# Kernel optimization log

Measured on AMD Instinct MI355X. Metric: run time of the kernel, lower is better.

## Reference

```python
import jax, jax.numpy as jnp
import numpy as np

D = 1024      # d_model
H = 16        # n_head
DH = D // H   # d_head = 64
DFF = 4 * D   # 4096
B, T = 1, 4096
EPS = 1e-5


def _layernorm(x, scale, bias):
    mu = jnp.mean(x, axis=-1, keepdims=True)
    var = jnp.mean(jnp.square(x - mu), axis=-1, keepdims=True)
    return (x - mu) * jax.lax.rsqrt(var + EPS) * scale + bias


def setup_inputs() -> dict:
    key = jax.random.key(0)
    ks = jax.random.split(key, 8)
    s = 0.02
    return {
        "x": jax.random.normal(ks[0], (B, T, D), jnp.float32),
        "ln1_scale": jnp.ones((D,), jnp.float32),
        "ln1_bias": jnp.zeros((D,), jnp.float32),
        "W_attn": jax.random.normal(ks[1], (D, 3 * D), jnp.float32) * s,
        "b_attn": jnp.zeros((3 * D,), jnp.float32),
        "W_proj": jax.random.normal(ks[2], (D, D), jnp.float32) * s,
        "b_proj": jnp.zeros((D,), jnp.float32),
        "ln2_scale": jnp.ones((D,), jnp.float32),
        "ln2_bias": jnp.zeros((D,), jnp.float32),
        "W_fc": jax.random.normal(ks[3], (D, DFF), jnp.float32) * s,
        "b_fc": jnp.zeros((DFF,), jnp.float32),
        "W_fc2": jax.random.normal(ks[4], (DFF, D), jnp.float32) * s,
        "b_fc2": jnp.zeros((D,), jnp.float32),
    }


def reference(x, ln1_scale, ln1_bias, W_attn, b_attn, W_proj, b_proj,
              ln2_scale, ln2_bias, W_fc, b_fc, W_fc2, b_fc2):
    Bx, Tx, C = x.shape
    # --- attention branch ---
    h = _layernorm(x, ln1_scale, ln1_bias)
    qkv = h @ W_attn + b_attn                      # [B,T,3D]
    q, k, v = jnp.split(qkv, 3, axis=-1)
    q = q.reshape(Bx, Tx, H, DH).transpose(0, 2, 1, 3)  # [B,H,T,dh]
    k = k.reshape(Bx, Tx, H, DH).transpose(0, 2, 1, 3)
    v = v.reshape(Bx, Tx, H, DH).transpose(0, 2, 1, 3)
    att = jnp.einsum('bhqd,bhkd->bhqk', q, k) * (1.0 / jnp.sqrt(DH))
    causal = jnp.tril(jnp.ones((Tx, Tx), dtype=jnp.bool_))[None, None]
    att = jnp.where(causal, att, -jnp.inf)
    att = jax.nn.softmax(att, axis=-1)
    y = jnp.einsum('bhqk,bhkd->bhqd', att, v)      # [B,H,T,dh]
    y = y.transpose(0, 2, 1, 3).reshape(Bx, Tx, C)
    y = y @ W_proj + b_proj
    x = x + y
    # --- MLP branch ---
    h2 = _layernorm(x, ln2_scale, ln2_bias)
    m = jax.nn.gelu(h2 @ W_fc + b_fc)              # approximate gelu (flax default)
    m = m @ W_fc2 + b_fc2
    return x + m
```

## Files before the change

kernel.cpp:

```cpp
#include <hip/hip_runtime.h>
#include <hip/hip_bf16.h>

typedef short bf16x8 __attribute__((ext_vector_type(8)));
typedef float f32x4 __attribute__((ext_vector_type(4)));
typedef unsigned short u16;
typedef unsigned int u32;

#define TSEQ 4096
#define DMODEL 1024
#define NHEAD 16
#define DHEAD 64
#define DFF 4096

__device__ __forceinline__ u16 f2bf(float f) {
    u32 u = __builtin_bit_cast(u32, f);
    u32 lsb = (u >> 16) & 1u;
    u += 0x7fffu + lsb;
    return (u16)(u >> 16);
}

__device__ __forceinline__ float exp2_hw(float x) {
    float r;
    asm("v_exp_f32 %0, %1" : "=v"(r) : "v"(x));
    return r;
}

__device__ __forceinline__ float rcp_hw(float x) {
    float r;
    asm("v_rcp_f32 %0, %1" : "=v"(r) : "v"(x));
    return r;
}

__device__ __forceinline__ u32 cvt_pk_bf16(float a, float b) {
    u32 r;
    asm("v_cvt_pk_bf16_f32 %0, %1, %2" : "=v"(r) : "v"(a), "v"(b));
    return r;
}

__device__ __forceinline__ void gload_lds16(const u16* g, u16* l) {
    __builtin_amdgcn_global_load_lds(
        (const __attribute__((address_space(1))) u32*)g,
        (__attribute__((address_space(3))) u32*)l, 16, 0, 0);
}

__device__ __forceinline__ void transpose_tile(
    const float* __restrict__ W, u16* __restrict__ Wt, int K, int N, int bx, int by,
    float (*tile)[65])
{
    const int t = threadIdx.x;
    const int c = t & 63, r4 = t >> 6;
    const int col0 = bx * 64;
    const int row0 = by * 64;
#pragma unroll
    for (int p = 0; p < 16; p++) {
        const int r = 4 * p + r4;
        tile[r][c] = W[(size_t)(row0 + r) * N + col0 + c];
    }
    __syncthreads();
#pragma unroll
    for (int p = 0; p < 16; p++) {
        const int r = 4 * p + r4;
        Wt[(size_t)(col0 + r) * K + row0 + c] = f2bf(tile[c][r]);
    }
}

__device__ __forceinline__ void ln_rows(
    const float* __restrict__ x, const float* __restrict__ sc,
    const float* __restrict__ bi, u16* __restrict__ out, int blk)
{
    const int lane = threadIdx.x & 63;
    const int row = blk * 4 + (threadIdx.x >> 6);
    const float* xr = x + (size_t)row * DMODEL;
    float4 v[4];
    float s = 0.f, s2 = 0.f;
#pragma unroll
    for (int q = 0; q < 4; q++) {
        v[q] = *(const float4*)(xr + 4 * (lane + 64 * q));
        s  += v[q].x + v[q].y + v[q].z + v[q].w;
        s2 += v[q].x * v[q].x + v[q].y * v[q].y + v[q].z * v[q].z + v[q].w * v[q].w;
    }
#pragma unroll
    for (int off = 1; off < 64; off <<= 1) {
        s  += __shfl_xor(s, off);
        s2 += __shfl_xor(s2, off);
    }
    const float mu = s * (1.f / DMODEL);
    const float rstd = rsqrtf(s2 * (1.f / DMODEL) - mu * mu + 1e-5f);
#pragma unroll
    for (int q = 0; q < 4; q++) {
        const int c = 4 * (lane + 64 * q);
        const float4 scv = *(const float4*)(sc + c);
        const float4 biv = *(const float4*)(bi + c);
        ushort4 ov;
        ov.x = f2bf((v[q].x - mu) * rstd * scv.x + biv.x);
        ov.y = f2bf((v[q].y - mu) * rstd * scv.y + biv.y);
        ov.z = f2bf((v[q].z - mu) * rstd * scv.z + biv.z);
        ov.w = f2bf((v[q].w - mu) * rstd * scv.w + biv.w);
        *(ushort4*)(out + (size_t)row * DMODEL + c) = ov;
    }
}

__global__ __launch_bounds__(256)
void prep_kernel(const float* __restrict__ x, const float* __restrict__ ln1_s,
                 const float* __restrict__ ln1_b, u16* __restrict__ h,
                 const float* __restrict__ W_attn, u16* __restrict__ WtAttn,
                 const float* __restrict__ W_proj, u16* __restrict__ WtProj,
                 const float* __restrict__ W_fc,   u16* __restrict__ WtFc,
                 const float* __restrict__ W_fc2,  u16* __restrict__ WtFc2)
{
    __shared__ float tile[64][65];
    int b = blockIdx.x;
    if (b < 1024) { ln_rows(x, ln1_s, ln1_b, h, b); return; }
    b -= 1024;
    if (b < 768)  { transpose_tile(W_attn, WtAttn, 1024, 3072, b % 48, b / 48, tile); return; }
    b -= 768;
    if (b < 256)  { transpose_tile(W_proj, WtProj, 1024, 1024, b % 16, b / 16, tile); return; }
    b -= 256;
    if (b < 1024) { transpose_tile(W_fc,   WtFc,   1024, 4096, b % 64, b / 64, tile); return; }
    b -= 1024;
    transpose_tile(W_fc2, WtFc2, 4096, 1024, b % 16, b / 16, tile);
}

__global__ __launch_bounds__(256)
void v_transpose_kernel(const u16* __restrict__ qkv, u16* __restrict__ Vtg)
{
    __shared__ u16 tile[64][72];
    const int t = threadIdx.x;
    const int hh = blockIdx.y, t0 = blockIdx.x * 64;
#pragma unroll
    for (int p = 0; p < 2; p++) {
        const int L = p * 2048 + t * 8;
        const int r = L >> 6, c = L & 63;
        const bf16x8 v = *(const bf16x8*)(qkv + (size_t)(t0 + r) * 3072 + 2048 + hh * 64 + c);
#pragma unroll
        for (int i = 0; i < 8; i++) tile[c + i][r] = (u16)v[i];
    }
    __syncthreads();
#pragma unroll
    for (int p = 0; p < 2; p++) {
        const int L = p * 2048 + t * 8;
        const int d = L >> 6, c = L & 63;
        bf16x8 v;
#pragma unroll
        for (int i = 0; i < 8; i++) v[i] = (short)tile[d][c + i];
        *(bf16x8*)(Vtg + (size_t)(hh * 64 + d) * TSEQ + t0 + c) = v;
    }
}

__global__ __launch_bounds__(256)
void ln_kernel(const float* __restrict__ x, const float* __restrict__ sc,
               const float* __restrict__ bi, u16* __restrict__ out)
{
    ln_rows(x, sc, bi, out, blockIdx.x);
}

template<int BN, int GELU_F, int OUT_BF16, int HAS_RES, int HAS_BIAS, int FUSE_Z1 = 0>
__global__ __launch_bounds__(256)
void gemm_kernel(const u16* __restrict__ A, int lda,
                 const u16* __restrict__ Bt, int ldb,
                 const float* __restrict__ bias, const float* __restrict__ res,
                 u16* __restrict__ outb, float* __restrict__ outf0,
                 float* __restrict__ outf1, int M, int N, int Kblk)
{
    constexpr int MI = (BN == 128) ? 4 : 2;
    __shared__ u16 Alds[128 * 64];
    __shared__ u16 Blds[BN * 64];
    const int t = threadIdx.x;
    const int lane = t & 63, w = t >> 6;
    const int g = lane >> 4, fr = lane & 15;
    const int m0 = blockIdx.y * 128, n0 = blockIdx.x * BN;
    const size_t koff = (size_t)blockIdx.z * Kblk;
    const int rowbase = (BN == 128) ? (w >> 1) * 64 : w * 32;
    const int colbase = (BN == 128) ? (w & 1) * 64 : 0;
    float* outf = blockIdx.z ? outf1 : outf0;

    f32x4 zero4 = {0.f, 0.f, 0.f, 0.f};
    f32x4 acc[MI][4];
#pragma unroll
    for (int i = 0; i < MI; i++)
#pragma unroll
        for (int j = 0; j < 4; j++) acc[i][j] = zero4;

    for (int k0 = 0; k0 < Kblk; k0 += 64) {
        __syncthreads();
#pragma unroll
        for (int p = 0; p < 4; p++) {
            const int c = p * 256 + t;
            const int r = c >> 3, j = (c & 7) ^ (r & 7);
            gload_lds16(A + (size_t)(m0 + r) * lda + koff + k0 + j * 8, Alds + c * 8);
        }
#pragma unroll
        for (int p = 0; p < (BN == 128 ? 4 : 2); p++) {
            const int c = p * 256 + t;
            const int r = c >> 3, j = (c & 7) ^ (r & 7);
            gload_lds16(Bt + (size_t)(n0 + r) * ldb + koff + k0 + j * 8, Blds + c * 8);
        }
        __syncthreads();

#pragma unroll
        for (int ks = 0; ks < 2; ks++) {
            bf16x8 af[MI], bfr[4];
#pragma unroll
            for (int i = 0; i < MI; i++)
                af[i] = *(const bf16x8*)(Alds + (rowbase + i * 16 + fr) * 64 + (((ks * 4 + g) ^ (fr & 7)) * 8));
#pragma unroll
            for (int j = 0; j < 4; j++)
                bfr[j] = *(const bf16x8*)(Blds + (colbase + j * 16 + fr) * 64 + (((ks * 4 + g) ^ (fr & 7)) * 8));
#pragma unroll
            for (int i = 0; i < MI; i++)
#pragma unroll
                for (int j = 0; j < 4; j++)
                    acc[i][j] = __builtin_amdgcn_mfma_f32_16x16x32_bf16(af[i], bfr[j], acc[i][j], 0, 0, 0);
        }
    }

    const bool fuse = FUSE_Z1 && (blockIdx.z == 1);
#pragma unroll
    for (int j = 0; j < 4; j++) {
        const int col = n0 + colbase + j * 16 + fr;
        float bv = 0.f;
        if (HAS_BIAS) bv = bias[col];
        if (FUSE_Z1 && fuse) bv = bias[col];
#pragma unroll
        for (int i = 0; i < MI; i++) {
#pragma unroll
            for (int r = 0; r < 4; r++) {
                const int row = m0 + rowbase + i * 16 + g * 4 + r;
                float v = acc[i][j][r] + bv;
                if (GELU_F) {
                    const float q = 0.7978845608028654f * (v + 0.044715f * v * v * v);
                    const float e = exp2_hw(fminf(q, 30.f) * 2.8853900817779268f);
                    v = v * e * rcp_hw(e + 1.0f);
                }
                if (HAS_RES) v += res[(size_t)row * N + col];
                if (FUSE_Z1 && fuse) v += res[(size_t)row * N + col];
                if (OUT_BF16) outb[(size_t)row * N + col] = f2bf(v);
                else          outf[(size_t)row * N + col] = v;
            }
        }
    }
}

__global__ __launch_bounds__(512, 2)
void gemm256_kernel(const u16* __restrict__ A, const u16* __restrict__ Bt,
                    const float* __restrict__ bias, u16* __restrict__ outb,
                    int M, int N, int K)
{
    __shared__ u16 Alds[256 * 64];
    __shared__ u16 Blds[128 * 64];
    const int t = threadIdx.x;
    const int lane = t & 63, w = t >> 6;
    const int g = lane >> 4, fr = lane & 15;
    const int m0 = blockIdx.y * 256, n0 = blockIdx.x * 128;
    const int rowbase = (w >> 1) * 64;
    const int colbase = (w & 1) * 64;

    f32x4 zero4 = {0.f, 0.f, 0.f, 0.f};
    f32x4 acc[4][4];
#pragma unroll
    for (int i = 0; i < 4; i++)
#pragma unroll
        for (int j = 0; j < 4; j++) acc[i][j] = zero4;

    for (int k0 = 0; k0 < K; k0 += 64) {
        __syncthreads();
#pragma unroll
        for (int p = 0; p < 4; p++) {
            const int c = p * 512 + t;
            const int r = c >> 3, j = (c & 7) ^ (r & 7);
            gload_lds16(A + (size_t)(m0 + r) * K + k0 + j * 8, Alds + c * 8);
        }
#pragma unroll
        for (int p = 0; p < 2; p++) {
            const int c = p * 512 + t;
            const int r = c >> 3, j = (c & 7) ^ (r & 7);
            gload_lds16(Bt + (size_t)(n0 + r) * K + k0 + j * 8, Blds + c * 8);
        }
        __syncthreads();

#pragma unroll
        for (int ks = 0; ks < 2; ks++) {
            bf16x8 af[4], bfr[4];
#pragma unroll
            for (int i = 0; i < 4; i++)
                af[i] = *(const bf16x8*)(Alds + (rowbase + i * 16 + fr) * 64 + (((ks * 4 + g) ^ (fr & 7)) * 8));
#pragma unroll
            for (int j = 0; j < 4; j++)
                bfr[j] = *(const bf16x8*)(Blds + (colbase + j * 16 + fr) * 64 + (((ks * 4 + g) ^ (fr & 7)) * 8));
#pragma unroll
            for (int i = 0; i < 4; i++)
#pragma unroll
                for (int j = 0; j < 4; j++)
                    acc[i][j] = __builtin_amdgcn_mfma_f32_16x16x32_bf16(af[i], bfr[j], acc[i][j], 0, 0, 0);
        }
    }

#pragma unroll
    for (int j = 0; j < 4; j++) {
        const int col = n0 + colbase + j * 16 + fr;
        const float bv = bias[col];
#pragma unroll
        for (int i = 0; i < 4; i++) {
#pragma unroll
            for (int r = 0; r < 4; r++) {
                const int row = m0 + rowbase + i * 16 + g * 4 + r;
                float v = acc[i][j][r] + bv;
                const float q = 0.7978845608028654f * (v + 0.044715f * v * v * v);
                const float e = exp2_hw(fminf(q, 30.f) * 2.8853900817779268f);
                v = v * e * rcp_hw(e + 1.0f);
                outb[(size_t)row * N + col] = f2bf(v);
            }
        }
    }
}

__global__ __launch_bounds__(256)
void fc2_merge_kernel(float* __restrict__ out, const float* __restrict__ part)
{
    const int i = blockIdx.x * 256 + threadIdx.x;
    const float4 o = ((const float4*)out)[i];
    const float4 p = ((const float4*)part)[i];
    float4 v;
    v.x = o.x + p.x;
    v.y = o.y + p.y;
    v.z = o.z + p.z;
    v.w = o.w + p.w;
    ((float4*)out)[i] = v;
}

__device__ __forceinline__ void softmax_update(
    const f32x4 st[4], bool diag, int klim, int g, int fr,
    float& mrow, float& lrow, f32x4 o[4], u16* Pl)
{
    const float ninf = -__builtin_inff();
    const float C = 0.125f * 1.4426950408889634f;
    float av[4][4];
#pragma unroll
    for (int ct = 0; ct < 4; ct++)
#pragma unroll
        for (int r = 0; r < 4; r++) {
            float aa = st[ct][r];
            if (diag && (ct * 16 + g * 4 + r) > klim) aa = ninf;
            av[ct][r] = aa;
        }
    float m0 = fmaxf(fmaxf(av[0][0], av[0][1]), fmaxf(av[0][2], av[0][3]));
    float m1 = fmaxf(fmaxf(av[1][0], av[1][1]), fmaxf(av[1][2], av[1][3]));
    float m2 = fmaxf(fmaxf(av[2][0], av[2][1]), fmaxf(av[2][2], av[2][3]));
    float m3 = fmaxf(fmaxf(av[3][0], av[3][1]), fmaxf(av[3][2], av[3][3]));
    float vm = fmaxf(fmaxf(m0, m1), fmaxf(m2, m3));
    vm = fmaxf(vm, __shfl_xor(vm, 16));
    vm = fmaxf(vm, __shfl_xor(vm, 32));
    const float mn = (vm <= mrow + 64.f) ? mrow : vm;
    const float mnC = mn * C;
    float rs = 0.f;
#pragma unroll
    for (int ct = 0; ct < 4; ct++) {
        const float p0 = exp2_hw(__builtin_fmaf(av[ct][0], C, -mnC));
        const float p1 = exp2_hw(__builtin_fmaf(av[ct][1], C, -mnC));
        const float p2 = exp2_hw(__builtin_fmaf(av[ct][2], C, -mnC));
        const float p3 = exp2_hw(__builtin_fmaf(av[ct][3], C, -mnC));
        rs += (p0 + p1) + (p2 + p3);
        uint2 pk;
        pk.x = cvt_pk_bf16(p0, p1);
        pk.y = cvt_pk_bf16(p2, p3);
        const int chunk = ct * 2 + (g >> 1);
        const int addr = fr * 64 + ((chunk ^ (fr & 7)) * 8) + (g & 1) * 4;
        *(uint2*)(Pl + addr) = pk;
    }
    rs += __shfl_xor(rs, 16);
    rs += __shfl_xor(rs, 32);
    const float sc = exp2_hw((mrow - mn) * C);
    lrow = __builtin_fmaf(lrow, sc, rs);
    const bool nores = (mn == mrow);
    mrow = mn;
    if (!__all(nores)) {
        float scb[4];
#pragma unroll
        for (int j = 0; j < 4; j++) scb[j] = __shfl(sc, g * 4 + j);
#pragma unroll
        for (int dt = 0; dt < 4; dt++)
#pragma unroll
            for (int j = 0; j < 4; j++) o[dt][j] *= scb[j];
    }
}

__global__ __launch_bounds__(512, 4)
void attn_kernel(const u16* __restrict__ qkv, const u16* __restrict__ Vtg,
                 u16* __restrict__ y)
{
    __shared__ u16 Klds[2][128 * 64];
    __shared__ u16 Vlds[2][64 * 128];
    __shared__ u16 Plds[8][16 * 64];
    const int t = threadIdx.x, lane = t & 63, w = t >> 6;
    const int g = lane >> 4, fr = lane & 15;
    const int wv = w & 3, grp = w >> 2;
    const int hh = blockIdx.y;
    const int ii = blockIdx.x;
    const int ntB = 64 - ii;
    const int qAw = ii * 64 + wv * 16;
    const int qBw = (63 - ii) * 64 + wv * 16;

    bf16x8 aqA[2], aqB[2];
#pragma unroll
    for (int s = 0; s < 2; s++) {
        aqA[s] = *(const bf16x8*)(qkv + (size_t)(qAw + fr) * 3072 + hh * 64 + s * 32 + g * 8);
        aqB[s] = *(const bf16x8*)(qkv + (size_t)(qBw + fr) * 3072 + hh * 64 + s * 32 + g * 8);
    }

    f32x4 zero4 = {0.f, 0.f, 0.f, 0.f};
    f32x4 oA[4] = {zero4, zero4, zero4, zero4};
    f32x4 oB[4] = {zero4, zero4, zero4, zero4};
    const float ninf = -__builtin_inff();
    float mA = ninf, lA = 0.f, mB = ninf, lB = 0.f;

    const int cK0 = t, cK1 = t + 512;
    const int rK0 = cK0 >> 3, jK0 = (cK0 & 7) ^ (rK0 & 7);
    const int rK1 = cK1 >> 3, jK1 = (cK1 & 7) ^ (rK1 & 7);
    const int rv0 = cK0 >> 4, cj0 = cK0 & 15;
    const int jv0 = (cj0 & 8) | ((cj0 & 7) ^ (rv0 & 7));
    const int rv1 = cK1 >> 4, cj1 = cK1 & 15;
    const int jv1 = (cj1 & 8) | ((cj1 & 7) ^ (rv1 & 7));
    const u16* gk0 = qkv + (size_t)rK0 * 3072 + 1024 + hh * 64 + jK0 * 8;
    const u16* gk1 = qkv + (size_t)rK1 * 3072 + 1024 + hh * 64 + jK1 * 8;
    const u16* gv0 = Vtg + (size_t)(hh * 64 + rv0) * TSEQ + jv0 * 8;
    const u16* gv1 = Vtg + (size_t)(hh * 64 + rv1) * TSEQ + jv1 * 8;

#define STAGE(buf, k0) do { \
        gload_lds16(gk0 + (size_t)(k0) * 3072, Klds[buf] + cK0 * 8); \
        gload_lds16(gk1 + (size_t)(k0) * 3072, Klds[buf] + cK1 * 8); \
        gload_lds16(gv0 + (k0), Vlds[buf] + cK0 * 8); \
        gload_lds16(gv1 + (k0), Vlds[buf] + cK1 * 8); \
    } while (0)

    const int nIter = (65 - ii) >> 1;
    STAGE(0, 0);

    int cur = 0;
    for (int j = 0; j < nIter; j++) {
        __syncthreads();
        if (j + 1 < nIter) STAGE(cur ^ 1, (j + 1) * 128);

        const int kt = 2 * j + grp;
        const bool aB = kt < ntB;
        const bool aA = kt <= ii;
        if (aB | aA) {
            const u16* Kl = Klds[cur] + grp * (64 * 64);
            const u16* Vl = Vlds[cur];
            const int klim = wv * 16 + fr;

            f32x4 stA[4] = {zero4, zero4, zero4, zero4};
            f32x4 stB[4] = {zero4, zero4, zero4, zero4};
#pragma unroll
            for (int ct = 0; ct < 4; ct++) {
#pragma unroll
                for (int ds = 0; ds < 2; ds++) {
                    const bf16x8 bk = *(const bf16x8*)(Kl + (ct * 16 + fr) * 64 + (((ds * 4 + g) ^ (fr & 7)) * 8));
                    if (aB) stB[ct] = __builtin_amdgcn_mfma_f32_16x16x32_bf16(bk, aqB[ds], stB[ct], 0, 0, 0);
                    if (aA) stA[ct] = __builtin_amdgcn_mfma_f32_16x16x32_bf16(bk, aqA[ds], stA[ct], 0, 0, 0);
                }
            }

            if (aB) {
                softmax_update(stB, kt == ntB - 1, klim, g, fr, mB, lB, oB, Plds[w]);
                __builtin_amdgcn_s_waitcnt(0xc07f);
#pragma unroll
                for (int kkh = 0; kkh < 2; kkh++) {
                    const bf16x8 pa = *(const bf16x8*)(&Plds[w][fr * 64 + (((kkh * 4 + g) ^ (fr & 7)) * 8)]);
#pragma unroll
                    for (int dt = 0; dt < 4; dt++) {
                        const int cc = grp * 8 + kkh * 4 + g;
                        const bf16x8 bv = *(const bf16x8*)(Vl + (dt * 16 + fr) * 128 + (((cc & 8) | ((cc & 7) ^ (fr & 7))) * 8));
                        oB[dt] = __builtin_amdgcn_mfma_f32_16x16x32_bf16(pa, bv, oB[dt], 0, 0, 0);
                    }
                }
            }
            if (aA) {
                softmax_update(stA, kt == ii, klim, g, fr, mA, lA, oA, Plds[w]);
                __builtin_amdgcn_s_waitcnt(0xc07f);
#pragma unroll
                for (int kkh = 0; kkh < 2; kkh++) {
                    const bf16x8 pa = *(const bf16x8*)(&Plds[w][fr * 64 + (((kkh * 4 + g) ^ (fr & 7)) * 8)]);
#pragma unroll
                    for (int dt = 0; dt < 4; dt++) {
                        const int cc = grp * 8 + kkh * 4 + g;
                        const bf16x8 bv = *(const bf16x8*)(Vl + (dt * 16 + fr) * 128 + (((cc & 8) | ((cc & 7) ^ (fr & 7))) * 8));
                        oA[dt] = __builtin_amdgcn_mfma_f32_16x16x32_bf16(pa, bv, oA[dt], 0, 0, 0);
                    }
                }
            }
        }
        cur ^= 1;
    }
#undef STAGE

    __syncthreads();
    float* Of = (float*)&Klds[0][0];
    float2* Ml = (float2*)&Vlds[0][0];
    const float C = 0.125f * 1.4426950408889634f;
    if (grp == 1) {
#pragma unroll
        for (int dt = 0; dt < 4; dt++)
#pragma unroll
            for (int jq = 0; jq < 4; jq++) {
                Of[((wv * 2 + 0) * 16 + g * 4 + jq) * 64 + dt * 16 + fr] = oA[dt][jq];
                Of[((wv * 2 + 1) * 16 + g * 4 + jq) * 64 + dt * 16 + fr] = oB[dt][jq];
            }
        if (g == 0) {
            Ml[(wv * 2 + 0) * 16 + fr] = make_float2(mA, lA);
            Ml[(wv * 2 + 1) * 16 + fr] = make_float2(mB, lB);
        }
    }
    __syncthreads();
    if (grp == 0) {
#pragma unroll
        for (int jq = 0; jq < 4; jq++) {
            {
                const float m0 = __shfl(mA, g * 4 + jq), l0 = __shfl(lA, g * 4 + jq);
                const float2 ml1 = Ml[(wv * 2 + 0) * 16 + g * 4 + jq];
                const float mm = fmaxf(m0, ml1.x);
                const float s0 = exp2_hw((m0 - mm) * C);
                const float s1 = exp2_hw((ml1.x - mm) * C);
                const float rl = rcp_hw(__builtin_fmaf(l0, s0, ml1.y * s1));
#pragma unroll
                for (int dt = 0; dt < 4; dt++) {
                    const float o1 = Of[((wv * 2 + 0) * 16 + g * 4 + jq) * 64 + dt * 16 + fr];
                    y[(size_t)(qAw + g * 4 + jq) * DMODEL + hh * 64 + dt * 16 + fr] =
                        f2bf((oA[dt][jq] * s0 + o1 * s1) * rl);
                }
            }
            {
                const float m0 = __shfl(mB, g * 4 + jq), l0 = __shfl(lB, g * 4 + jq);
                const float2 ml1 = Ml[(wv * 2 + 1) * 16 + g * 4 + jq];
                const float mm = fmaxf(m0, ml1.x);
                const float s0 = exp2_hw((m0 - mm) * C);
                const float s1 = exp2_hw((ml1.x - mm) * C);
                const float rl = rcp_hw(__builtin_fmaf(l0, s0, ml1.y * s1));
#pragma unroll
                for (int dt = 0; dt < 4; dt++) {
                    const float o1 = Of[((wv * 2 + 1) * 16 + g * 4 + jq) * 64 + dt * 16 + fr];
                    y[(size_t)(qBw + g * 4 + jq) * DMODEL + hh * 64 + dt * 16 + fr] =
                        f2bf((oB[dt][jq] * s0 + o1 * s1) * rl);
                }
            }
        }
    }
}

extern "C" void kernel_launch(void* const* d_in, const int* in_sizes, int n_in,
                              void* d_out, int out_size, void* d_ws, size_t ws_size,
                              hipStream_t stream)
{
    const float* x      = (const float*)d_in[0];
    const float* ln1_s  = (const float*)d_in[1];
    const float* ln1_b  = (const float*)d_in[2];
    const float* W_attn = (const float*)d_in[3];
    const float* b_attn = (const float*)d_in[4];
    const float* W_proj = (const float*)d_in[5];
    const float* b_proj = (const float*)d_in[6];
    const float* ln2_s  = (const float*)d_in[7];
    const float* ln2_b  = (const float*)d_in[8];
    const float* W_fc   = (const float*)d_in[9];
    const float* b_fc   = (const float*)d_in[10];
    const float* W_fc2  = (const float*)d_in[11];
    const float* b_fc2  = (const float*)d_in[12];
    float* out = (float*)d_out;

    char* ws = (char*)d_ws;
    u16* WtAttn = (u16*)ws; ws += (size_t)3072 * 1024 * 2;
    u16* WtProj = (u16*)ws; ws += (size_t)1024 * 1024 * 2;
    u16* WtFc   = (u16*)ws; ws += (size_t)4096 * 1024 * 2;
    u16* WtFc2  = (u16*)ws; ws += (size_t)1024 * 4096 * 2;
    u16* bufA   = (u16*)ws; ws += (size_t)4096 * 1024 * 2;
    u16* bufB   = (u16*)ws; ws += (size_t)4096 * 4096 * 2;
    float* x1   = (float*)ws; ws += (size_t)4096 * 1024 * 4;
    u16* Vtg    = (u16*)x1;
    float* P0   = (float*)d_ws;

    prep_kernel<<<4096, 256, 0, stream>>>(x, ln1_s, ln1_b, bufA,
                                          W_attn, WtAttn, W_proj, WtProj,
                                          W_fc, WtFc, W_fc2, WtFc2);

    gemm_kernel<128, 0, 1, 0, 1><<<dim3(24, 32, 1), 256, 0, stream>>>(
        bufA, 1024, WtAttn, 1024, b_attn, nullptr, bufB, nullptr, nullptr, 4096, 3072, 1024);
    v_transpose_kernel<<<dim3(TSEQ / 64, NHEAD), 256, 0, stream>>>(bufB, Vtg);
    attn_kernel<<<dim3(32, NHEAD), 512, 0, stream>>>(bufB, Vtg, bufA);
    gemm_kernel<64, 0, 0, 1, 1><<<dim3(16, 32, 1), 256, 0, stream>>>(
        bufA, 1024, WtProj, 1024, b_proj, x, nullptr, x1, nullptr, 4096, 1024, 1024);

    ln_kernel<<<TSEQ / 4, 256, 0, stream>>>(x1, ln2_s, ln2_b, bufA);
    gemm256_kernel<<<dim3(32, 16), 512, 0, stream>>>(
        bufA, WtFc, b_fc, bufB, 4096, 4096, 1024);
    gemm_kernel<128, 0, 0, 0, 0, 1><<<dim3(8, 32, 2), 256, 0, stream>>>(
        bufB, 4096, WtFc2, 4096, b_fc2, x1, nullptr, P0, out, 4096, 1024, 2048);
    fc2_merge_kernel<<<4096, 256, 0, stream>>>(out, P0);
}
```

Baseline: 280.9 us.

## Split-K the output projection, fuse merge into LN2, add MFMA priority hints

The output projection GEMM now uses 128-wide tiles with a two-way split-K. One partial goes into x1 together with the residual and bias, and the other goes into a scratch buffer. A new ln_merge kernel adds the two partials, writes x1 back, and computes the second layernorm in one pass using a single-pass mean and variance. In the attention kernel, causal masking is moved out of the softmax so it only runs on diagonal tiles, and s_setprio raises wave priority around the MFMA sections. This trades extra partial-buffer traffic for better CU occupancy on the projection GEMM, and the single-pass variance can lose some numerical precision.

```diff
diff --git a/kernel.cpp b/kernel.cpp
--- a/kernel.cpp
+++ b/kernel.cpp
@@ -148,10 +148,46 @@
 }
 
 __global__ __launch_bounds__(256)
-void ln_kernel(const float* __restrict__ x, const float* __restrict__ sc,
-               const float* __restrict__ bi, u16* __restrict__ out)
-{
-    ln_rows(x, sc, bi, out, blockIdx.x);
+void ln_merge_kernel(float* __restrict__ x1, const float* __restrict__ part,
+                     const float* __restrict__ sc, const float* __restrict__ bi,
+                     u16* __restrict__ out)
+{
+    const int lane = threadIdx.x & 63;
+    const int row = blockIdx.x * 4 + (threadIdx.x >> 6);
+    float* xr = x1 + (size_t)row * DMODEL;
+    const float* pr = part + (size_t)row * DMODEL;
+    float4 v[4];
+    float s = 0.f, s2 = 0.f;
+#pragma unroll
+    for (int q = 0; q < 4; q++) {
+        const int c = 4 * (lane + 64 * q);
+        const float4 a = *(const float4*)(xr + c);
+        const float4 p = *(const float4*)(pr + c);
+        v[q].x = a.x + p.x; v[q].y = a.y + p.y;
+        v[q].z = a.z + p.z; v[q].w = a.w + p.w;
+        *(float4*)(xr + c) = v[q];
+        s  += v[q].x + v[q].y + v[q].z + v[q].w;
+        s2 += v[q].x * v[q].x + v[q].y * v[q].y + v[q].z * v[q].z + v[q].w * v[q].w;
+    }
+#pragma unroll
+    for (int off = 1; off < 64; off <<= 1) {
+        s  += __shfl_xor(s, off);
+        s2 += __shfl_xor(s2, off);
+    }
+    const float mu = s * (1.f / DMODEL);
+    const float rstd = rsqrtf(s2 * (1.f / DMODEL) - mu * mu + 1e-5f);
+#pragma unroll
+    for (int q = 0; q < 4; q++) {
+        const int c = 4 * (lane + 64 * q);
+        const float4 scv = *(const float4*)(sc + c);
+        const float4 biv = *(const float4*)(bi + c);
+        ushort4 ov;
+        ov.x = f2bf((v[q].x - mu) * rstd * scv.x + biv.x);
+        ov.y = f2bf((v[q].y - mu) * rstd * scv.y + biv.y);
+        ov.z = f2bf((v[q].z - mu) * rstd * scv.z + biv.z);
+        ov.w = f2bf((v[q].w - mu) * rstd * scv.w + biv.w);
+        *(ushort4*)(out + (size_t)row * DMODEL + c) = ov;
+    }
 }
 
 template<int BN, int GELU_F, int OUT_BF16, int HAS_RES, int HAS_BIAS, int FUSE_Z1 = 0>
@@ -328,25 +364,25 @@
     ((float4*)out)[i] = v;
 }
 
+__device__ __forceinline__ void mask_diag(f32x4 st[4], int klim, int g)
+{
+    const float ninf = -__builtin_inff();
+#pragma unroll
+    for (int ct = 0; ct < 4; ct++)
+#pragma unroll
+        for (int r = 0; r < 4; r++)
+            if (ct * 16 + g * 4 + r > klim) st[ct][r] = ninf;
+}
+
 __device__ __forceinline__ void softmax_update(
-    const f32x4 st[4], bool diag, int klim, int g, int fr,
+    const f32x4 st[4], int g, int fr,
     float& mrow, float& lrow, f32x4 o[4], u16* Pl)
 {
-    const float ninf = -__builtin_inff();
     const float C = 0.125f * 1.4426950408889634f;
-    float av[4][4];
-#pragma unroll
-    for (int ct = 0; ct < 4; ct++)
-#pragma unroll
-        for (int r = 0; r < 4; r++) {
-            float aa = st[ct][r];
-            if (diag && (ct * 16 + g * 4 + r) > klim) aa = ninf;
-            av[ct][r] = aa;
-        }
-    float m0 = fmaxf(fmaxf(av[0][0], av[0][1]), fmaxf(av[0][2], av[0][3]));
-    float m1 = fmaxf(fmaxf(av[1][0], av[1][1]), fmaxf(av[1][2], av[1][3]));
-    float m2 = fmaxf(fmaxf(av[2][0], av[2][1]), fmaxf(av[2][2], av[2][3]));
-    float m3 = fmaxf(fmaxf(av[3][0], av[3][1]), fmaxf(av[3][2], av[3][3]));
+    float m0 = fmaxf(fmaxf(st[0][0], st[0][1]), fmaxf(st[0][2], st[0][3]));
+    float m1 = fmaxf(fmaxf(st[1][0], st[1][1]), fmaxf(st[1][2], st[1][3]));
+    float m2 = fmaxf(fmaxf(st[2][0], st[2][1]), fmaxf(st[2][2], st[2][3]));
+    float m3 = fmaxf(fmaxf(st[3][0], st[3][1]), fmaxf(st[3][2], st[3][3]));
     float vm = fmaxf(fmaxf(m0, m1), fmaxf(m2, m3));
     vm = fmaxf(vm, __shfl_xor(vm, 16));
     vm = fmaxf(vm, __shfl_xor(vm, 32));
@@ -355,10 +391,10 @@
     float rs = 0.f;
 #pragma unroll
     for (int ct = 0; ct < 4; ct++) {
-        const float p0 = exp2_hw(__builtin_fmaf(av[ct][0], C, -mnC));
-        const float p1 = exp2_hw(__builtin_fmaf(av[ct][1], C, -mnC));
-        const float p2 = exp2_hw(__builtin_fmaf(av[ct][2], C, -mnC));
-        const float p3 = exp2_hw(__builtin_fmaf(av[ct][3], C, -mnC));
+        const float p0 = exp2_hw(__builtin_fmaf(st[ct][0], C, -mnC));
+        const float p1 = exp2_hw(__builtin_fmaf(st[ct][1], C, -mnC));
+        const float p2 = exp2_hw(__builtin_fmaf(st[ct][2], C, -mnC));
+        const float p3 = exp2_hw(__builtin_fmaf(st[ct][3], C, -mnC));
         rs += (p0 + p1) + (p2 + p3);
         uint2 pk;
         pk.x = cvt_pk_bf16(p0, p1);
@@ -450,6 +486,7 @@
 
             f32x4 stA[4] = {zero4, zero4, zero4, zero4};
             f32x4 stB[4] = {zero4, zero4, zero4, zero4};
+            __builtin_amdgcn_s_setprio(1);
 #pragma unroll
             for (int ct = 0; ct < 4; ct++) {
 #pragma unroll
@@ -459,10 +496,13 @@
                     if (aA) stA[ct] = __builtin_amdgcn_mfma_f32_16x16x32_bf16(bk, aqA[ds], stA[ct], 0, 0, 0);
                 }
             }
+            __builtin_amdgcn_s_setprio(0);
 
             if (aB) {
-                softmax_update(stB, kt == ntB - 1, klim, g, fr, mB, lB, oB, Plds[w]);
+                if (kt == ntB - 1) mask_diag(stB, klim, g);
+                softmax_update(stB, g, fr, mB, lB, oB, Plds[w]);
                 __builtin_amdgcn_s_waitcnt(0xc07f);
+                __builtin_amdgcn_s_setprio(1);
 #pragma unroll
                 for (int kkh = 0; kkh < 2; kkh++) {
                     const bf16x8 pa = *(const bf16x8*)(&Plds[w][fr * 64 + (((kkh * 4 + g) ^ (fr & 7)) * 8)]);
@@ -473,10 +513,13 @@
                         oB[dt] = __builtin_amdgcn_mfma_f32_16x16x32_bf16(pa, bv, oB[dt], 0, 0, 0);
                     }
                 }
+                __builtin_amdgcn_s_setprio(0);
             }
             if (aA) {
-                softmax_update(stA, kt == ii, klim, g, fr, mA, lA, oA, Plds[w]);
+                if (kt == ii) mask_diag(stA, klim, g);
+                softmax_update(stA, g, fr, mA, lA, oA, Plds[w]);
                 __builtin_amdgcn_s_waitcnt(0xc07f);
+                __builtin_amdgcn_s_setprio(1);
 #pragma unroll
                 for (int kkh = 0; kkh < 2; kkh++) {
                     const bf16x8 pa = *(const bf16x8*)(&Plds[w][fr * 64 + (((kkh * 4 + g) ^ (fr & 7)) * 8)]);
@@ -487,6 +530,7 @@
                         oA[dt] = __builtin_amdgcn_mfma_f32_16x16x32_bf16(pa, bv, oA[dt], 0, 0, 0);
                     }
                 }
+                __builtin_amdgcn_s_setprio(0);
             }
         }
         cur ^= 1;
@@ -575,6 +619,7 @@
     float* x1   = (float*)ws; ws += (size_t)4096 * 1024 * 4;
     u16* Vtg    = (u16*)x1;
     float* P0   = (float*)d_ws;
+    float* P1   = (float*)bufB;
 
     prep_kernel<<<4096, 256, 0, stream>>>(x, ln1_s, ln1_b, bufA,
                                           W_attn, WtAttn, W_proj, WtProj,
@@ -584,10 +629,10 @@
         bufA, 1024, WtAttn, 1024, b_attn, nullptr, bufB, nullptr, nullptr, 4096, 3072, 1024);
     v_transpose_kernel<<<dim3(TSEQ / 64, NHEAD), 256, 0, stream>>>(bufB, Vtg);
     attn_kernel<<<dim3(32, NHEAD), 512, 0, stream>>>(bufB, Vtg, bufA);
-    gemm_kernel<64, 0, 0, 1, 1><<<dim3(16, 32, 1), 256, 0, stream>>>(
-        bufA, 1024, WtProj, 1024, b_proj, x, nullptr, x1, nullptr, 4096, 1024, 1024);
-
-    ln_kernel<<<TSEQ / 4, 256, 0, stream>>>(x1, ln2_s, ln2_b, bufA);
+    gemm_kernel<128, 0, 0, 0, 0, 1><<<dim3(8, 32, 2), 256, 0, stream>>>(
+        bufA, 1024, WtProj, 1024, b_proj, x, nullptr, P1, x1, 4096, 1024, 512);
+
+    ln_merge_kernel<<<1024, 256, 0, stream>>>(x1, P1, ln2_s, ln2_b, bufA);
     gemm256_kernel<<<dim3(32, 16), 512, 0, stream>>>(
         bufA, WtFc, b_fc, bufB, 4096, 4096, 1024);
     gemm_kernel<128, 0, 0, 0, 0, 1><<<dim3(8, 32, 2), 256, 0, stream>>>(
```

Result: slower. 840.1 us (+199.1%).
